# Kernel optimization log

Measured on AMD Instinct MI355X. Metric: run time of the kernel, lower is better.

The kernel has to match this reference:

```python
import jax, jax.numpy as jnp
import numpy as np

B, S, E, H = 2, 2048, 1024, 16
D = E // H  # head dim = 64


def setup_inputs() -> dict:
    key = jax.random.key(0)
    ks = jax.random.split(key, 6)
    x = jax.random.normal(ks[0], (B, S, E), dtype=jnp.float32)
    attn_mask = jax.random.bernoulli(ks[1], 0.1, (B, S, S))  # True = masked
    scale = 1.0 / np.sqrt(E)
    w_kernel = jax.random.normal(ks[2], (E, 3 * E), dtype=jnp.float32) * scale
    w_bias = jax.random.normal(ks[3], (3 * E,), dtype=jnp.float32) * 0.02
    fc_kernel = jax.random.normal(ks[4], (E, E), dtype=jnp.float32) * scale
    fc_bias = jax.random.normal(ks[5], (E,), dtype=jnp.float32) * 0.02
    return {"x": x, "attn_mask": attn_mask, "w_kernel": w_kernel,
            "w_bias": w_bias, "fc_kernel": fc_kernel, "fc_bias": fc_bias}


def reference(x, attn_mask, w_kernel, w_bias, fc_kernel, fc_bias):
    b, s, e = x.shape
    qkv = jnp.einsum("bse,ef->bsf", x, w_kernel) + w_bias  # (B,S,3E)
    q, k, v = jnp.split(qkv, 3, axis=-1)

    def heads(t):  # (B,S,E) -> (B,H,S,D)
        return t.reshape(b, s, H, D).transpose(0, 2, 1, 3)

    q, k, v = heads(q), heads(k), heads(v)
    scores = jnp.einsum("bhqd,bhkd->bhqk", q, k) / jnp.sqrt(jnp.float32(D))
    # faithful quirk: masked positions are filled with 1e-9, not -inf
    scores = jnp.where(attn_mask[:, None, :, :], jnp.float32(1e-9), scores)
    A = jax.nn.softmax(scores, axis=-1)
    out = jnp.einsum("bhqk,bhkd->bhqd", A, v)  # (B,H,S,D)
    out = out.transpose(0, 2, 1, 3).reshape(b, s, e)
    # dropout is identity in eval mode
    return jnp.einsum("bse,ef->bsf", out, fc_kernel) + fc_bias
```

## Files before the change

### kernel.cpp

```cpp
#include <hip/hip_runtime.h>
#include <math.h>

#define BB 2
#define SS 2048
#define EE 1024
#define HH 16

typedef _Float16 f16;
typedef __attribute__((ext_vector_type(8))) _Float16 f16x8;
typedef __attribute__((ext_vector_type(4))) _Float16 f16x4;
typedef __attribute__((ext_vector_type(2))) _Float16 f16x2;
typedef __attribute__((ext_vector_type(4))) float f32x4;

union P8 { f16x8 v8; f16x2 h2[4]; };
union V8 { f16x8 v8; f16x4 v4[2]; };

#define QSCALE 0.18033688011112042f

#if __has_builtin(__builtin_amdgcn_exp2f)
#define EXP2(x) __builtin_amdgcn_exp2f(x)
#else
#define EXP2(x) exp2f(x)
#endif

static __device__ __forceinline__ f16x2 pk2(float a, float b) {
#if __has_builtin(__builtin_amdgcn_cvt_pkrtz)
  return __builtin_bit_cast(f16x2, __builtin_amdgcn_cvt_pkrtz(a, b));
#else
  f16x2 r; r[0] = (f16)a; r[1] = (f16)b; return r;
#endif
}

static __device__ __forceinline__ void gl16(const void* g, void* l) {
  __builtin_amdgcn_global_load_lds(
      (const __attribute__((address_space(1))) void*)g,
      (__attribute__((address_space(3))) void*)l, 16, 0, 0);
}

__global__ __launch_bounds__(256) void prep(
    const float* __restrict__ x, f16* __restrict__ xh,
    const float* __restrict__ wk, f16* __restrict__ Wt,
    const float* __restrict__ fck, f16* __restrict__ fckT,
    const int* __restrict__ mask, unsigned long long* __restrict__ mbits)
{
  const int bid = blockIdx.x;
  const int tid = threadIdx.x;
  __shared__ float T[64][65];

  if (bid < 2048) {
    const int i = (bid * 256 + tid) * 8;
    float4 a = *(const float4*)(x + i);
    float4 b = *(const float4*)(x + i + 4);
    f16x8 o;
    o[0] = (f16)a.x; o[1] = (f16)a.y; o[2] = (f16)a.z; o[3] = (f16)a.w;
    o[4] = (f16)b.x; o[5] = (f16)b.y; o[6] = (f16)b.z; o[7] = (f16)b.w;
    *(f16x8*)(xh + i) = o;
    return;
  }
  if (bid < 3072) {
    const float* in; f16* outp; int K, N, bx, by;
    if (bid < 2816) {
      const int lb = bid - 2048;
      bx = lb % 48; by = lb / 48; in = wk; outp = Wt; K = 1024; N = 3072;
    } else {
      const int lb = bid - 2816;
      bx = lb & 15; by = lb >> 4; in = fck; outp = fckT; K = 1024; N = 1024;
    }
    const int k0 = by * 64, n0 = bx * 64;
    const int tr = tid >> 4, tc = (tid & 15) * 4;
#pragma unroll
    for (int i = 0; i < 4; ++i) {
      int r = tr + i * 16;
      *(float4*)&T[r][tc] = *(const float4*)(in + (size_t)(k0 + r) * N + n0 + tc);
    }
    __syncthreads();
#pragma unroll
    for (int i = 0; i < 4; ++i) {
      int nl = tr + i * 16;
      f16x4 v;
      v[0] = (f16)T[tc + 0][nl];
      v[1] = (f16)T[tc + 1][nl];
      v[2] = (f16)T[tc + 2][nl];
      v[3] = (f16)T[tc + 3][nl];
      *(f16x4*)(outp + (size_t)(n0 + nl) * K + k0 + tc) = v;
    }
    return;
  }
  const int lb = bid - 3072;
  const int wg = lb * 4 + (tid >> 6);
  const int lane = tid & 63;
  const size_t base = (size_t)wg * 256;
#pragma unroll
  for (int k = 0; k < 4; ++k) {
    const unsigned long long bal = __ballot(mask[base + k * 64 + lane] != 0);
    if (lane == 0) mbits[(base >> 6) + k] = bal;
  }
}

__global__ __launch_bounds__(256) void gemm_qkv(
    const f16* __restrict__ A, const f16* __restrict__ Bt,
    const float* __restrict__ bias,
    f16* __restrict__ oQK, f16* __restrict__ oVT)
{
  __shared__ f16 SH[8192];
  f16* Ah = SH;
  f16* Bh = SH + 4096;
  const int K = 1024;

  const int t = threadIdx.x;
  const int l = t & 63, w = t >> 6;
  const int l15 = l & 15, l4 = l >> 4;
  const int wr = w >> 1, wc = w & 1;
  const int n0 = blockIdx.x * 128, m0 = blockIdx.y * 128;

  const int srow = l >> 2;
  const int gch  = (l & 3) ^ (srow & 3);
  const f16* Ap0 = A + (size_t)(m0 + w * 32 + srow) * K + gch * 8;
  const f16* Ap1 = Ap0 + (size_t)16 * K;
  const f16* Bp0 = Bt + (size_t)(n0 + w * 32 + srow) * K + gch * 8;
  const f16* Bp1 = Bp0 + (size_t)16 * K;
  f16* ldsA0 = &Ah[(w * 32) * 32];
  f16* ldsA1 = &Ah[(w * 32 + 16) * 32];
  f16* ldsB0 = &Bh[(w * 32) * 32];
  f16* ldsB1 = &Bh[(w * 32 + 16) * 32];

  f32x4 acc[4][4] = {};
  const int csw = (l15 & 3);

  for (int k0 = 0; k0 < K; k0 += 32) {
    gl16(Ap0 + k0, ldsA0);
    gl16(Ap1 + k0, ldsA1);
    gl16(Bp0 + k0, ldsB0);
    gl16(Bp1 + k0, ldsB1);
    __syncthreads();

    f16x8 af[4], bf[4];
#pragma unroll
    for (int mr = 0; mr < 4; ++mr) {
      const int row = wr * 64 + mr * 16 + l15;
      af[mr] = *(const f16x8*)&Ah[row * 32 + ((l4 ^ csw) * 8)];
    }
#pragma unroll
    for (int nr = 0; nr < 4; ++nr) {
      const int row = wc * 64 + nr * 16 + l15;
      bf[nr] = *(const f16x8*)&Bh[row * 32 + ((l4 ^ csw) * 8)];
    }
    __builtin_amdgcn_s_setprio(1);
#pragma unroll
    for (int mr = 0; mr < 4; ++mr)
#pragma unroll
      for (int nr = 0; nr < 4; ++nr)
        acc[mr][nr] = __builtin_amdgcn_mfma_f32_16x16x32_f16(
            af[mr], bf[nr], acc[mr][nr], 0, 0, 0);
    __builtin_amdgcn_s_setprio(0);
    __syncthreads();
  }

  if (n0 < 2048) {
    const float qs = (n0 < 1024) ? QSCALE : 1.0f;
#pragma unroll
    for (int half = 0; half < 2; ++half) {
      __syncthreads();
      if (wr == half) {
#pragma unroll
        for (int nr = 0; nr < 4; ++nr) {
          const int col = wc * 64 + nr * 16 + l15;
          const float bv = bias[n0 + col];
#pragma unroll
          for (int mr = 0; mr < 4; ++mr)
#pragma unroll
            for (int j = 0; j < 4; ++j) {
              const int r = mr * 16 + l4 * 4 + j;
              SH[r * 128 + ((((col >> 3) ^ (r & 15)) << 3) | (col & 7))] =
                  (f16)((acc[mr][nr][j] + bv) * qs);
            }
        }
      }
      __syncthreads();
#pragma unroll
      for (int cc = 0; cc < 4; ++cc) {
        const int row = w * 16 + cc * 4 + (l >> 4);
        const int ch  = l & 15;
        const f16x8 v =
            *(const f16x8*)&SH[row * 128 + ((ch ^ (row & 15)) << 3)];
        *(f16x8*)(oQK + (size_t)(m0 + half * 64 + row) * 2048 + n0 + ch * 8) = v;
      }
    }
  } else {
#pragma unroll
    for (int nr = 0; nr < 4; ++nr) {
      const int n = n0 + wc * 64 + nr * 16 + l15;
      const float bv = bias[n];
      const int hh = (n - 2048) >> 6;
      const int d = (n - 2048) & 63;
#pragma unroll
      for (int mr = 0; mr < 4; ++mr) {
        const int tok0 = m0 + wr * 64 + mr * 16 + l4 * 4;
        const int bq = tok0 >> 11, sq = tok0 & 2047;
        f16x4 v;
        v[0] = (f16)(acc[mr][nr][0] + bv);
        v[1] = (f16)(acc[mr][nr][1] + bv);
        v[2] = (f16)(acc[mr][nr][2] + bv);
        v[3] = (f16)(acc[mr][nr][3] + bv);
        *(f16x4*)(oVT + ((size_t)(bq * 16 + hh) * 64 + d) * SS + sq) = v;
      }
    }
  }
}

__global__ __launch_bounds__(256) void gemm_fc(
    const f16* __restrict__ A, const f16* __restrict__ Bt,
    const float* __restrict__ bias, float* __restrict__ outF)
{
  __shared__ f16 Ah[128 * 32];
  __shared__ f16 Bh[64 * 32];
  const int K = 1024, N = 1024;

  const int t = threadIdx.x;
  const int l = t & 63, w = t >> 6;
  const int l15 = l & 15, l4 = l >> 4;
  const int wr = w >> 1, wc = w & 1;
  const int n0 = blockIdx.x * 64, m0 = blockIdx.y * 128;

  const int srow = l >> 2;
  const int gch  = (l & 3) ^ (srow & 3);
  const f16* Ap0 = A + (size_t)(m0 + w * 32 + srow) * K + gch * 8;
  const f16* Ap1 = Ap0 + (size_t)16 * K;
  const f16* Bp0 = Bt + (size_t)(n0 + w * 16 + srow) * K + gch * 8;
  f16* ldsA0 = &Ah[(w * 32) * 32];
  f16* ldsA1 = &Ah[(w * 32 + 16) * 32];
  f16* ldsB0 = &Bh[(w * 16) * 32];

  f32x4 acc[4][2] = {};
  const int csw = (l15 & 3);

  for (int k0 = 0; k0 < K; k0 += 32) {
    gl16(Ap0 + k0, ldsA0);
    gl16(Ap1 + k0, ldsA1);
    gl16(Bp0 + k0, ldsB0);
    __syncthreads();

    f16x8 af[4], bf[2];
#pragma unroll
    for (int mr = 0; mr < 4; ++mr) {
      const int row = wr * 64 + mr * 16 + l15;
      af[mr] = *(const f16x8*)&Ah[row * 32 + ((l4 ^ csw) * 8)];
    }
#pragma unroll
    for (int nr = 0; nr < 2; ++nr) {
      const int row = wc * 32 + nr * 16 + l15;
      bf[nr] = *(const f16x8*)&Bh[row * 32 + ((l4 ^ csw) * 8)];
    }
    __builtin_amdgcn_s_setprio(1);
#pragma unroll
    for (int mr = 0; mr < 4; ++mr)
#pragma unroll
      for (int nr = 0; nr < 2; ++nr)
        acc[mr][nr] = __builtin_amdgcn_mfma_f32_16x16x32_f16(
            af[mr], bf[nr], acc[mr][nr], 0, 0, 0);
    __builtin_amdgcn_s_setprio(0);
    __syncthreads();
  }

#pragma unroll
  for (int nr = 0; nr < 2; ++nr) {
    const int n = n0 + wc * 32 + nr * 16 + l15;
    const float bv = bias[n];
#pragma unroll
    for (int mr = 0; mr < 4; ++mr)
#pragma unroll
      for (int j = 0; j < 4; ++j) {
        const int m = m0 + wr * 64 + mr * 16 + l4 * 4 + j;
        outF[(size_t)m * N + n] = acc[mr][nr][j] + bv;
      }
  }
}

#define VPAD 36
__global__ __launch_bounds__(256, 4) void attn_mfma(
    const f16* __restrict__ qkbuf, const f16* __restrict__ vT,
    const unsigned long long* __restrict__ mbits,
    f16* __restrict__ Opart, float* __restrict__ Lpart)
{
  __shared__ f16 Kds[2][32 * 64];
  __shared__ f16 Vds[2][64 * VPAD];

  const int t = threadIdx.x;
  const int w = t >> 6, l = t & 63, l15 = l & 15, l4 = l >> 4;
  const int bh = blockIdx.y, b = bh >> 4, h = bh & 15;
  const int ks = blockIdx.z;
  const int qbase = blockIdx.x * 128 + w * 32;

  f16x8 q00, q01, q10, q11;
  {
    const size_t r0 = (size_t)(b * SS + qbase + l15) * 2048 + h * 64;
    const size_t r1 = (size_t)(b * SS + qbase + 16 + l15) * 2048 + h * 64;
    q00 = *(const f16x8*)(qkbuf + r0 + l4 * 8);
    q01 = *(const f16x8*)(qkbuf + r0 + 32 + l4 * 8);
    q10 = *(const f16x8*)(qkbuf + r1 + l4 * 8);
    q11 = *(const f16x8*)(qkbuf + r1 + 32 + l4 * 8);
  }

  f32x4 accA[4] = {}, accB[4] = {};
  f32x4 accLA = {}, accLB = {};
  f16x8 ones;
#pragma unroll
  for (int i = 0; i < 8; ++i) ones[i] = (f16)1.0f;

  const unsigned int* mA =
      (const unsigned int*)mbits + (size_t)(b * SS + qbase + l15) * 64 + ks * 32;
  const unsigned int* mB =
      (const unsigned int*)mbits + (size_t)(b * SS + qbase + 16 + l15) * 64 + ks * 32;

  const int srow = t >> 3;
  const int scb  = (t & 7) * 8;
  const int sws  = (srow & 7) << 3;
  const f16* kb = qkbuf + (size_t)b * SS * 2048 + 1024 + h * 64 + scb +
                  (size_t)ks * 1024 * 2048;
  const int vd  = t >> 2;
  const int vkb = (t & 3) * 8;
  const f16* vb = vT + ((size_t)bh * 64 + vd) * SS + ks * 1024 + vkb;

  f16x8 kr0; V8 vr0;
#define LOADT(kt)                                                         \
  {                                                                       \
    kr0 = *(const f16x8*)(kb + (size_t)((kt) + srow) * 2048);             \
    vr0.v8 = *(const f16x8*)(vb + (kt));                                  \
  }
#define COMMIT(bi)                                                        \
  {                                                                       \
    *(f16x8*)&Kds[bi][srow * 64 + (scb ^ sws)] = kr0;                     \
    *(f16x4*)&Vds[bi][vd * VPAD + vkb]     = vr0.v4[0];                   \
    *(f16x4*)&Vds[bi][vd * VPAD + vkb + 4] = vr0.v4[1];                   \
  }

  LOADT(0)
  COMMIT(0)
  LOADT(32)
  __syncthreads();

  const int swr = (l15 & 7) << 3;

#define BODY(cur, tI)                                                         \
  {                                                                           \
    const unsigned int mbA = mA[tI];                                          \
    const unsigned int mbB = mB[tI];                                          \
    float pA[8], pB[8];                                                       \
    _Pragma("unroll")                                                         \
    for (int g = 0; g < 2; ++g) {                                             \
      const f16* krow = &Kds[cur][(g * 16 + l15) * 64];                       \
      const f16x8 k0 = *(const f16x8*)(krow + ((l4 * 8) ^ swr));              \
      const f16x8 k1 = *(const f16x8*)(krow + ((32 + l4 * 8) ^ swr));         \
      __builtin_amdgcn_s_setprio(1);                                          \
      f32x4 SA = __builtin_amdgcn_mfma_f32_16x16x32_f16(                      \
          k0, q00, (f32x4){0.f, 0.f, 0.f, 0.f}, 0, 0, 0);                     \
      SA = __builtin_amdgcn_mfma_f32_16x16x32_f16(k1, q01, SA, 0, 0, 0);      \
      f32x4 SB = __builtin_amdgcn_mfma_f32_16x16x32_f16(                      \
          k0, q10, (f32x4){0.f, 0.f, 0.f, 0.f}, 0, 0, 0);                     \
      SB = __builtin_amdgcn_mfma_f32_16x16x32_f16(k1, q11, SB, 0, 0, 0);      \
      __builtin_amdgcn_s_setprio(0);                                          \
      const unsigned int nibA = mbA >> (g * 16 + l4 * 4);                     \
      const unsigned int nibB = mbB >> (g * 16 + l4 * 4);                     \
      _Pragma("unroll")                                                       \
      for (int j = 0; j < 4; ++j) {                                           \
        pA[g * 4 + j] = ((nibA >> j) & 1u) ? 1.0f : EXP2(SA[j]);              \
        pB[g * 4 + j] = ((nibB >> j) & 1u) ? 1.0f : EXP2(SB[j]);              \
      }                                                                       \
    }                                                                         \
    P8 uA, uB;                                                                \
    uA.h2[0] = pk2(pA[0], pA[1]); uA.h2[1] = pk2(pA[2], pA[3]);               \
    uA.h2[2] = pk2(pA[4], pA[5]); uA.h2[3] = pk2(pA[6], pA[7]);               \
    uB.h2[0] = pk2(pB[0], pB[1]); uB.h2[1] = pk2(pB[2], pB[3]);               \
    uB.h2[2] = pk2(pB[4], pB[5]); uB.h2[3] = pk2(pB[6], pB[7]);               \
    __builtin_amdgcn_s_setprio(1);                                            \
    _Pragma("unroll")                                                         \
    for (int dg = 0; dg < 4; ++dg) {                                          \
      const f16* vrow = &Vds[cur][(dg * 16 + l15) * VPAD];                    \
      V8 uv;                                                                  \
      uv.v4[0] = *(const f16x4*)(vrow + l4 * 4);                              \
      uv.v4[1] = *(const f16x4*)(vrow + 16 + l4 * 4);                         \
      accA[dg] = __builtin_amdgcn_mfma_f32_16x16x32_f16(uA.v8, uv.v8,         \
                                                        accA[dg], 0, 0, 0);   \
      accB[dg] = __builtin_amdgcn_mfma_f32_16x16x32_f16(uB.v8, uv.v8,         \
                                                        accB[dg], 0, 0, 0);   \
    }                                                                         \
    accLA = __builtin_amdgcn_mfma_f32_16x16x32_f16(uA.v8, ones, accLA,        \
                                                   0, 0, 0);                  \
    accLB = __builtin_amdgcn_mfma_f32_16x16x32_f16(uB.v8, ones, accLB,        \
                                                   0, 0, 0);                  \
    __builtin_amdgcn_s_setprio(0);                                            \
    if ((tI) + 1 < 32) {                                                      \
      COMMIT((cur) ^ 1)                                                       \
      if ((tI) + 2 < 32) LOADT(((tI) + 2) * 32)                               \
    }                                                                         \
    __syncthreads();                                                          \
  }

  for (int tI = 0; tI < 32; tI += 2) {
    BODY(0, tI)
    BODY(1, tI + 1)
  }

  const size_t obase = (size_t)ks * 4096 * EE;
#pragma unroll
  for (int j = 0; j < 4; ++j) {
    const int qr = l4 * 4 + j;
    const size_t rowA = (size_t)(b * SS + qbase + qr) * EE + h * 64 + l15;
    const size_t rowB = (size_t)(b * SS + qbase + 16 + qr) * EE + h * 64 + l15;
#pragma unroll
    for (int dg = 0; dg < 4; ++dg) {
      Opart[obase + rowA + dg * 16] = (f16)accA[dg][j];
      Opart[obase + rowB + dg * 16] = (f16)accB[dg][j];
    }
    if (l15 == 0) {
      Lpart[(size_t)ks * 4096 * HH + (size_t)(b * SS + qbase + qr) * HH + h] =
          accLA[j];
      Lpart[(size_t)ks * 4096 * HH +
            (size_t)(b * SS + qbase + 16 + qr) * HH + h] = accLB[j];
    }
  }
}

__global__ __launch_bounds__(256) void combine(
    const f16* __restrict__ Opart, const float* __restrict__ Lpart,
    f16* __restrict__ aout)
{
  const size_t i = ((size_t)blockIdx.x * 256 + threadIdx.x) * 8;
  const int token = (int)(i >> 10);
  const int h = (int)((i >> 6) & 15);
  const float inv =
      1.0f / (Lpart[(size_t)token * HH + h] +
              Lpart[(size_t)4096 * HH + (size_t)token * HH + h]);
  const f16x8 o0 = *(const f16x8*)(Opart + i);
  const f16x8 o1 = *(const f16x8*)(Opart + (size_t)4096 * EE + i);
  f16x8 o;
#pragma unroll
  for (int j = 0; j < 8; ++j)
    o[j] = (f16)(((float)o0[j] + (float)o1[j]) * inv);
  *(f16x8*)(aout + i) = o;
}

extern "C" void kernel_launch(void* const* d_in, const int* in_sizes, int n_in,
                              void* d_out, int out_size, void* d_ws,
                              size_t ws_size, hipStream_t stream)
{
  (void)in_sizes; (void)n_in; (void)out_size; (void)ws_size;
  const float* x   = (const float*)d_in[0];
  const int* mask  = (const int*)d_in[1];
  const float* wk  = (const float*)d_in[2];
  const float* wb  = (const float*)d_in[3];
  const float* fck = (const float*)d_in[4];
  const float* fcb = (const float*)d_in[5];
  float* out       = (float*)d_out;

  char* ws = (char*)d_ws;
  f16* fckT = (f16*)(ws);
  f16* qk   = (f16*)(ws + 2097152);
  f16* vT   = (f16*)(ws + 18874368);
  unsigned long long* mbits = (unsigned long long*)(ws + 27262976);
  float* Lp = (float*)(ws + 28311552);
  char* scratch = ws + 28835840;
  f16* xh    = (f16*)scratch;
  f16* Wt    = (f16*)(scratch + 8388608);
  f16* Opart = (f16*)scratch;
  f16* aoutH = qk;

  prep<<<11264, 256, 0, stream>>>(x, xh, wk, Wt, fck, fckT, mask, mbits);

  gemm_qkv<<<dim3(3072 / 128, 4096 / 128), 256, 0, stream>>>(
      xh, Wt, wb, qk, vT);

  attn_mfma<<<dim3(SS / 128, BB * HH, 2), 256, 0, stream>>>(
      qk, vT, mbits, Opart, Lp);
  combine<<<4096 * 1024 / (8 * 256), 256, 0, stream>>>(Opart, Lp, aoutH);

  gemm_fc<<<dim3(1024 / 64, 4096 / 128), 256, 0, stream>>>(
      aoutH, fckT, fcb, out);
}
```

Baseline: 237.5 us.

## Double-buffer LDS in QKV and FC GEMMs, swizzle block order, stage V-transpose stores

Both GEMM kernels now use two LDS buffers, so the global-to-LDS load for the next K tile is issued before the MFMAs on the current tile. That removes one barrier per iteration and overlaps memory latency with compute. Block indices are remapped with an XCD-style swizzle (bid&7) to improve L2 locality across the chiplets. The V-transpose epilogue now stages results through LDS so it can write 16-byte coalesced rows instead of scattered 8-byte stores. In exchange, LDS use doubles per block, which may lower occupancy.

```diff
diff --git a/kernel.cpp b/kernel.cpp
--- a/kernel.cpp
+++ b/kernel.cpp
@@ -102,16 +102,18 @@
     const float* __restrict__ bias,
     f16* __restrict__ oQK, f16* __restrict__ oVT)
 {
-  __shared__ f16 SH[8192];
-  f16* Ah = SH;
-  f16* Bh = SH + 4096;
+  __shared__ f16 SH[16384];
+
   const int K = 1024;
-
   const int t = threadIdx.x;
   const int l = t & 63, w = t >> 6;
   const int l15 = l & 15, l4 = l >> 4;
   const int wr = w >> 1, wc = w & 1;
-  const int n0 = blockIdx.x * 128, m0 = blockIdx.y * 128;
+
+  const int bid = blockIdx.x;
+  const int swz = (bid & 7) * 96 + (bid >> 3);
+  const int bx = swz % 24, by = swz / 24;
+  const int n0 = bx * 128, m0 = by * 128;
 
   const int srow = l >> 2;
   const int gch  = (l & 3) ^ (srow & 3);
@@ -119,48 +121,58 @@
   const f16* Ap1 = Ap0 + (size_t)16 * K;
   const f16* Bp0 = Bt + (size_t)(n0 + w * 32 + srow) * K + gch * 8;
   const f16* Bp1 = Bp0 + (size_t)16 * K;
-  f16* ldsA0 = &Ah[(w * 32) * 32];
-  f16* ldsA1 = &Ah[(w * 32 + 16) * 32];
-  f16* ldsB0 = &Bh[(w * 32) * 32];
-  f16* ldsB1 = &Bh[(w * 32 + 16) * 32];
+  const int offA0 = (w * 32) * 32, offA1 = (w * 32 + 16) * 32;
 
   f32x4 acc[4][4] = {};
   const int csw = (l15 & 3);
 
-  for (int k0 = 0; k0 < K; k0 += 32) {
-    gl16(Ap0 + k0, ldsA0);
-    gl16(Ap1 + k0, ldsA1);
-    gl16(Bp0 + k0, ldsB0);
-    gl16(Bp1 + k0, ldsB1);
-    __syncthreads();
-
-    f16x8 af[4], bf[4];
-#pragma unroll
-    for (int mr = 0; mr < 4; ++mr) {
-      const int row = wr * 64 + mr * 16 + l15;
-      af[mr] = *(const f16x8*)&Ah[row * 32 + ((l4 ^ csw) * 8)];
-    }
-#pragma unroll
-    for (int nr = 0; nr < 4; ++nr) {
-      const int row = wc * 64 + nr * 16 + l15;
-      bf[nr] = *(const f16x8*)&Bh[row * 32 + ((l4 ^ csw) * 8)];
-    }
-    __builtin_amdgcn_s_setprio(1);
-#pragma unroll
-    for (int mr = 0; mr < 4; ++mr)
-#pragma unroll
-      for (int nr = 0; nr < 4; ++nr)
-        acc[mr][nr] = __builtin_amdgcn_mfma_f32_16x16x32_f16(
-            af[mr], bf[nr], acc[mr][nr], 0, 0, 0);
-    __builtin_amdgcn_s_setprio(0);
-    __syncthreads();
+#define QSTAGE(bi, kt)                                                    \
+  {                                                                       \
+    f16* ab = SH + (bi) * 4096;                                           \
+    f16* bb = SH + 8192 + (bi) * 4096;                                    \
+    gl16(Ap0 + (kt) * 32, ab + offA0);                                    \
+    gl16(Ap1 + (kt) * 32, ab + offA1);                                    \
+    gl16(Bp0 + (kt) * 32, bb + offA0);                                    \
+    gl16(Bp1 + (kt) * 32, bb + offA1);                                    \
+  }
+
+#define QITER(bi, kt)                                                     \
+  {                                                                       \
+    if ((kt) + 1 < 32) QSTAGE((bi) ^ 1, (kt) + 1)                         \
+    const f16* ab = SH + (bi) * 4096;                                     \
+    const f16* bb = SH + 8192 + (bi) * 4096;                              \
+    f16x8 af[4], bf[4];                                                   \
+    _Pragma("unroll")                                                     \
+    for (int mr = 0; mr < 4; ++mr)                                        \
+      af[mr] = *(const f16x8*)&ab[(wr * 64 + mr * 16 + l15) * 32 +        \
+                                  ((l4 ^ csw) * 8)];                      \
+    _Pragma("unroll")                                                     \
+    for (int nr = 0; nr < 4; ++nr)                                        \
+      bf[nr] = *(const f16x8*)&bb[(wc * 64 + nr * 16 + l15) * 32 +        \
+                                  ((l4 ^ csw) * 8)];                      \
+    __builtin_amdgcn_s_setprio(1);                                        \
+    _Pragma("unroll")                                                     \
+    for (int mr = 0; mr < 4; ++mr)                                        \
+      _Pragma("unroll")                                                   \
+      for (int nr = 0; nr < 4; ++nr)                                      \
+        acc[mr][nr] = __builtin_amdgcn_mfma_f32_16x16x32_f16(             \
+            af[mr], bf[nr], acc[mr][nr], 0, 0, 0);                        \
+    __builtin_amdgcn_s_setprio(0);                                        \
+    __syncthreads();                                                      \
+  }
+
+  QSTAGE(0, 0)
+  __syncthreads();
+  for (int kt = 0; kt < 32; kt += 2) {
+    QITER(0, kt)
+    QITER(1, kt + 1)
   }
 
   if (n0 < 2048) {
     const float qs = (n0 < 1024) ? QSCALE : 1.0f;
 #pragma unroll
     for (int half = 0; half < 2; ++half) {
-      __syncthreads();
+      if (half) __syncthreads();
       if (wr == half) {
 #pragma unroll
         for (int nr = 0; nr < 4; ++nr) {
@@ -187,22 +199,34 @@
       }
     }
   } else {
-#pragma unroll
-    for (int nr = 0; nr < 4; ++nr) {
-      const int n = n0 + wc * 64 + nr * 16 + l15;
-      const float bv = bias[n];
-      const int hh = (n - 2048) >> 6;
-      const int d = (n - 2048) & 63;
-#pragma unroll
-      for (int mr = 0; mr < 4; ++mr) {
-        const int tok0 = m0 + wr * 64 + mr * 16 + l4 * 4;
-        const int bq = tok0 >> 11, sq = tok0 & 2047;
-        f16x4 v;
-        v[0] = (f16)(acc[mr][nr][0] + bv);
-        v[1] = (f16)(acc[mr][nr][1] + bv);
-        v[2] = (f16)(acc[mr][nr][2] + bv);
-        v[3] = (f16)(acc[mr][nr][3] + bv);
-        *(f16x4*)(oVT + ((size_t)(bq * 16 + hh) * 64 + d) * SS + sq) = v;
+    const int vbase = n0 - 2048;
+    const int bq = m0 >> 11, sq0 = m0 & 2047;
+#pragma unroll
+    for (int half = 0; half < 2; ++half) {
+      if (half) __syncthreads();
+      if (wc == half) {
+#pragma unroll
+        for (int nr = 0; nr < 4; ++nr) {
+          const int colh = nr * 16 + l15;
+          const float bv = bias[2048 + vbase + half * 64 + colh];
+#pragma unroll
+          for (int mr = 0; mr < 4; ++mr)
+#pragma unroll
+            for (int j = 0; j < 4; ++j) {
+              const int tok = wr * 64 + mr * 16 + l4 * 4 + j;
+              SH[colh * 136 + tok] = (f16)(acc[mr][nr][j] + bv);
+            }
+        }
+      }
+      __syncthreads();
+#pragma unroll
+      for (int u = 0; u < 4; ++u) {
+        const int unit = u * 256 + t;
+        const int colh = unit >> 4, ch = unit & 15;
+        const f16x8 v = *(const f16x8*)&SH[colh * 136 + ch * 8];
+        const int nloc = vbase + half * 64 + colh;
+        const int hh = nloc >> 6, d = nloc & 63;
+        *(f16x8*)(oVT + ((size_t)(bq * 16 + hh) * 64 + d) * SS + sq0 + ch * 8) = v;
       }
     }
   }
@@ -212,54 +236,69 @@
     const f16* __restrict__ A, const f16* __restrict__ Bt,
     const float* __restrict__ bias, float* __restrict__ outF)
 {
-  __shared__ f16 Ah[128 * 32];
-  __shared__ f16 Bh[64 * 32];
+  __shared__ f16 SH2[12288];
+
   const int K = 1024, N = 1024;
-
   const int t = threadIdx.x;
   const int l = t & 63, w = t >> 6;
   const int l15 = l & 15, l4 = l >> 4;
   const int wr = w >> 1, wc = w & 1;
-  const int n0 = blockIdx.x * 64, m0 = blockIdx.y * 128;
+
+  const int bid = blockIdx.x;
+  const int swz = (bid & 7) * 64 + (bid >> 3);
+  const int bx = swz & 15, by = swz >> 4;
+  const int n0 = bx * 64, m0 = by * 128;
 
   const int srow = l >> 2;
   const int gch  = (l & 3) ^ (srow & 3);
   const f16* Ap0 = A + (size_t)(m0 + w * 32 + srow) * K + gch * 8;
   const f16* Ap1 = Ap0 + (size_t)16 * K;
   const f16* Bp0 = Bt + (size_t)(n0 + w * 16 + srow) * K + gch * 8;
-  f16* ldsA0 = &Ah[(w * 32) * 32];
-  f16* ldsA1 = &Ah[(w * 32 + 16) * 32];
-  f16* ldsB0 = &Bh[(w * 16) * 32];
+  const int offA0 = (w * 32) * 32, offA1 = (w * 32 + 16) * 32;
+  const int offB0 = (w * 16) * 32;
 
   f32x4 acc[4][2] = {};
   const int csw = (l15 & 3);
 
-  for (int k0 = 0; k0 < K; k0 += 32) {
-    gl16(Ap0 + k0, ldsA0);
-    gl16(Ap1 + k0, ldsA1);
-    gl16(Bp0 + k0, ldsB0);
-    __syncthreads();
-
-    f16x8 af[4], bf[2];
-#pragma unroll
-    for (int mr = 0; mr < 4; ++mr) {
-      const int row = wr * 64 + mr * 16 + l15;
-      af[mr] = *(const f16x8*)&Ah[row * 32 + ((l4 ^ csw) * 8)];
-    }
-#pragma unroll
-    for (int nr = 0; nr < 2; ++nr) {
-      const int row = wc * 32 + nr * 16 + l15;
-      bf[nr] = *(const f16x8*)&Bh[row * 32 + ((l4 ^ csw) * 8)];
-    }
-    __builtin_amdgcn_s_setprio(1);
-#pragma unroll
-    for (int mr = 0; mr < 4; ++mr)
-#pragma unroll
-      for (int nr = 0; nr < 2; ++nr)
-        acc[mr][nr] = __builtin_amdgcn_mfma_f32_16x16x32_f16(
-            af[mr], bf[nr], acc[mr][nr], 0, 0, 0);
-    __builtin_amdgcn_s_setprio(0);
-    __syncthreads();
+#define FSTAGE(bi, kt)                                                    \
+  {                                                                       \
+    f16* ab = SH2 + (bi) * 4096;                                          \
+    f16* bb = SH2 + 8192 + (bi) * 2048;                                   \
+    gl16(Ap0 + (kt) * 32, ab + offA0);                                    \
+    gl16(Ap1 + (kt) * 32, ab + offA1);                                    \
+    gl16(Bp0 + (kt) * 32, bb + offB0);                                    \
+  }
+
+#define FITER(bi, kt)                                                     \
+  {                                                                       \
+    if ((kt) + 1 < 32) FSTAGE((bi) ^ 1, (kt) + 1)                         \
+    const f16* ab = SH2 + (bi) * 4096;                                    \
+    const f16* bb = SH2 + 8192 + (bi) * 2048;                             \
+    f16x8 af[4], bf[2];                                                   \
+    _Pragma("unroll")                                                     \
+    for (int mr = 0; mr < 4; ++mr)                                        \
+      af[mr] = *(const f16x8*)&ab[(wr * 64 + mr * 16 + l15) * 32 +        \
+                                  ((l4 ^ csw) * 8)];                      \
+    _Pragma("unroll")                                                     \
+    for (int nr = 0; nr < 2; ++nr)                                        \
+      bf[nr] = *(const f16x8*)&bb[(wc * 32 + nr * 16 + l15) * 32 +        \
+                                  ((l4 ^ csw) * 8)];                      \
+    __builtin_amdgcn_s_setprio(1);                                        \
+    _Pragma("unroll")                                                     \
+    for (int mr = 0; mr < 4; ++mr)                                        \
+      _Pragma("unroll")                                                   \
+      for (int nr = 0; nr < 2; ++nr)                                      \
+        acc[mr][nr] = __builtin_amdgcn_mfma_f32_16x16x32_f16(             \
+            af[mr], bf[nr], acc[mr][nr], 0, 0, 0);                        \
+    __builtin_amdgcn_s_setprio(0);                                        \
+    __syncthreads();                                                      \
+  }
+
+  FSTAGE(0, 0)
+  __syncthreads();
+  for (int kt = 0; kt < 32; kt += 2) {
+    FITER(0, kt)
+    FITER(1, kt + 1)
   }
 
 #pragma unroll
@@ -467,13 +506,11 @@
 
   prep<<<11264, 256, 0, stream>>>(x, xh, wk, Wt, fck, fckT, mask, mbits);
 
-  gemm_qkv<<<dim3(3072 / 128, 4096 / 128), 256, 0, stream>>>(
-      xh, Wt, wb, qk, vT);
+  gemm_qkv<<<768, 256, 0, stream>>>(xh, Wt, wb, qk, vT);
 
   attn_mfma<<<dim3(SS / 128, BB * HH, 2), 256, 0, stream>>>(
       qk, vT, mbits, Opart, Lp);
   combine<<<4096 * 1024 / (8 * 256), 256, 0, stream>>>(Opart, Lp, aoutH);
 
-  gemm_fc<<<dim3(1024 / 64, 4096 / 128), 256, 0, stream>>>(
-      aoutH, fckT, fcb, out);
-}
+  gemm_fc<<<512, 256, 0, stream>>>(aoutH, fckT, fcb, out);
+}
```

Result: no change. 233.9 us (-1.5%).
